# Performance work log

Hardware: AMD Instinct MI355X
Metric: run time of the kernel (lower is better)

## Reference

```python
import jax, jax.numpy as jnp
import numpy as np

N_NODES = 100000


def _sage_conv(x, src, dst, Wl, b, Wr):
    """PyG SAGEConv with mean aggregation: lin_l(mean_{j->i} x_j) + lin_r(x_i)."""
    msg = x[src]  # [E, d] gather of source-node features
    s = jax.ops.segment_sum(msg, dst, num_segments=N_NODES)  # [N, d]
    deg = jax.ops.segment_sum(jnp.ones_like(dst, dtype=x.dtype), dst,
                              num_segments=N_NODES)  # [N]
    mean = s / jnp.maximum(deg, 1.0)[:, None]  # nodes with no in-edges -> 0
    return mean @ Wl.T + b + x @ Wr.T


def setup_inputs() -> dict:
    key = jax.random.key(0)
    ks = jax.random.split(key, 12)
    in_f, h_f, out_f = 64, 64, 32
    E_half = 800000
    x = jax.random.normal(ks[0], (N_NODES, in_f), dtype=jnp.float32)
    edge_index1 = jax.random.randint(ks[1], (2, E_half), 0, N_NODES, dtype=jnp.int64)
    edge_weight1 = jax.random.uniform(ks[2], (E_half,), dtype=jnp.float32)
    edge_index2 = jax.random.randint(ks[3], (2, E_half), 0, N_NODES, dtype=jnp.int64)
    edge_weight2 = jax.random.uniform(ks[4], (E_half,), dtype=jnp.float32)
    s1 = 1.0 / np.sqrt(in_f)
    s2 = 1.0 / np.sqrt(h_f)
    W1l = jax.random.uniform(ks[5], (h_f, in_f), minval=-s1, maxval=s1, dtype=jnp.float32)
    b1 = jax.random.uniform(ks[6], (h_f,), minval=-s1, maxval=s1, dtype=jnp.float32)
    W1r = jax.random.uniform(ks[7], (h_f, in_f), minval=-s1, maxval=s1, dtype=jnp.float32)
    W2l = jax.random.uniform(ks[8], (out_f, h_f), minval=-s2, maxval=s2, dtype=jnp.float32)
    b2 = jax.random.uniform(ks[9], (out_f,), minval=-s2, maxval=s2, dtype=jnp.float32)
    W2r = jax.random.uniform(ks[10], (out_f, h_f), minval=-s2, maxval=s2, dtype=jnp.float32)
    return {"x": x, "edge_index1": edge_index1, "edge_weight1": edge_weight1,
            "edge_index2": edge_index2, "edge_weight2": edge_weight2,
            "W1l": W1l, "b1": b1, "W1r": W1r, "W2l": W2l, "b2": b2, "W2r": W2r}


def reference(x, edge_index1, edge_weight1, edge_index2, edge_weight2,
              W1l, b1, W1r, W2l, b2, W2r):
    # concat adjacency lists (edge_weight is concatenated but unused by SAGEConv)
    edge_index = jnp.concatenate([edge_index1, edge_index2], axis=-1)
    _edge_weight = jnp.concatenate([edge_weight1, edge_weight2], axis=-1)  # unused
    src, dst = edge_index[0], edge_index[1]
    # F.dropout with training=False -> identity (eval-mode reference)
    h = _sage_conv(x, src, dst, W1l, b1, W1r)
    h = jax.nn.relu(h)
    out = _sage_conv(h, src, dst, W2l, b2, W2r)
    return out
```

## Files before the change

### kernel.cpp

```cpp
#include <hip/hip_runtime.h>


constexpr int N_NODES = 100000;
constexpr int E_HALF  = 800000;
constexpr int E_TOT   = 2 * E_HALF;
constexpr int CAP     = 64;
constexpr int OVF_CAP = 4096;
constexpr int NB      = 200;
constexpr int NPB     = 500;
constexpr int BCAP    = 12288;
constexpr int EPB_A   = 2048;
constexpr int EPT_A   = EPB_A / 256;
constexpr int BINA_BLKS   = (E_TOT + EPB_A - 1) / EPB_A;
constexpr int CONV_BLKS   = N_NODES * 64 / 4 / 256;
constexpr int WSPLIT_BLKS = 48;

typedef short  s16x8 __attribute__((ext_vector_type(8)));
typedef float  f32x4 __attribute__((ext_vector_type(4)));
typedef unsigned short u16;

__device__ inline float bf(u16 u) { return __uint_as_float(((unsigned)u) << 16); }
__device__ inline u16 f2bf(float v) {
    unsigned b = __float_as_uint(v);
    b += 0x7FFFu + ((b >> 16) & 1u);
    return (u16)(b >> 16);
}
__device__ inline void acc4(float* s, uint2 v) {
    s[0] += __uint_as_float(v.x << 16);
    s[1] += __uint_as_float(v.x & 0xFFFF0000u);
    s[2] += __uint_as_float(v.y << 16);
    s[3] += __uint_as_float(v.y & 0xFFFF0000u);
}

__global__ __launch_bounds__(256) void binA_kernel(
    const int* __restrict__ ei1, const int* __restrict__ ei2,
    const float* __restrict__ x, u16* __restrict__ xb,
    const float* __restrict__ W1l, const float* __restrict__ W1r,
    const float* __restrict__ W2l, const float* __restrict__ W2r,
    short* __restrict__ B1hi, short* __restrict__ B1lo,
    short* __restrict__ B2hi, short* __restrict__ B2lo,
    uint2* __restrict__ barr, int* __restrict__ bcur,
    int* __restrict__ ovfA_cnt, int* __restrict__ ovfA)
{
    __shared__ int   hist[NB], base[NB], cur[NB], lofs[NB];
    __shared__ int   scan[256];
    __shared__ int   aux[EPB_A];
    __shared__ uint2 staged[EPB_A];
    int tid = threadIdx.x;

    if (blockIdx.x >= BINA_BLKS) {
        int bx = blockIdx.x - BINA_BLKS;
        if (bx < CONV_BLKS) {
            int i = bx * 256 + tid;
            float4 v = ((const float4*)x)[i];
            ushort4 rr;
            rr.x = f2bf(v.x); rr.y = f2bf(v.y);
            rr.z = f2bf(v.z); rr.w = f2bf(v.w);
            ((ushort4*)xb)[i] = rr;
        } else {
            int i = (bx - CONV_BLKS) * 256 + tid;
            float v; short* ph; short* pl; int idx;
            if (i < 64 * 128) {
                int o = i >> 7, k = i & 127;
                v = (k < 64) ? W1l[o * 64 + k] : W1r[o * 64 + (k - 64)];
                ph = B1hi; pl = B1lo; idx = i;
            } else {
                int j = i - 64 * 128;
                int o = j >> 6, k = j & 63;
                v = (o < 32) ? W2l[o * 64 + k] : W2r[(o - 32) * 64 + k];
                ph = B2hi; pl = B2lo; idx = j;
            }
            unsigned b  = __float_as_uint(v);
            float    hf = __uint_as_float(b & 0xFFFF0000u);
            float    r  = v - hf;
            ph[idx] = (short)(b >> 16);
            pl[idx] = (short)(__float_as_uint(r) >> 16);
        }
        return;
    }

    for (int t = tid; t < NB; t += 256) { hist[t] = 0; cur[t] = 0; }
    __syncthreads();

    int e0 = blockIdx.x * EPB_A;
    uint2 myE[EPT_A];
    int   myB[EPT_A];
    #pragma unroll
    for (int k = 0; k < EPT_A; k++) {
        int e = e0 + k * 256 + tid;
        myB[k] = -1;
        if (e < E_TOT) {
            const int* ei = (e < E_HALF) ? ei1 : ei2;
            int ee = (e < E_HALF) ? e : e - E_HALF;
            int dst = ei[E_HALF + ee];
            int src = ei[ee];
            myE[k] = make_uint2((unsigned)src, (unsigned)dst);
            myB[k] = dst / NPB;
            atomicAdd(&hist[myB[k]], 1);
        }
    }
    __syncthreads();

    int v = (tid < NB) ? hist[tid] : 0;
    scan[tid] = v;
    __syncthreads();
    #pragma unroll
    for (int off = 1; off < 256; off <<= 1) {
        int u = (tid >= off) ? scan[tid - off] : 0;
        __syncthreads();
        scan[tid] += u;
        __syncthreads();
    }
    if (tid < NB) lofs[tid] = scan[tid] - v;
    if (tid < NB) base[tid] = atomicAdd(&bcur[tid], hist[tid]);
    __syncthreads();

    #pragma unroll
    for (int k = 0; k < EPT_A; k++) {
        int b = myB[k];
        if (b < 0) continue;
        int rank = atomicAdd(&cur[b], 1);
        int p    = lofs[b] + rank;
        int gpos = base[b] + rank;
        if (gpos < BCAP) {
            staged[p] = myE[k];
            aux[p]    = b * BCAP + gpos;
        } else {
            aux[p] = -1;
            int o = atomicAdd(ovfA_cnt, 1);
            if (o < OVF_CAP) {
                ovfA[2 * o] = (int)myE[k].x; ovfA[2 * o + 1] = (int)myE[k].y;
            }
        }
    }
    __syncthreads();

    int tot = scan[255];
    for (int i = tid; i < tot; i += 256) {
        int a = aux[i];
        if (a >= 0) barr[a] = staged[i];
    }
}

__global__ __launch_bounds__(1024) void binB_kernel(
    const uint2* __restrict__ barr, const int* __restrict__ bcur,
    const int* __restrict__ ovfA_cnt, const int* __restrict__ ovfA,
    int* __restrict__ cnt, int* __restrict__ slots,
    int* __restrict__ ovfB_cnt, int* __restrict__ ovfB)
{
    __shared__ int lcnt[NPB];
    int tid = threadIdx.x, b = blockIdx.x;
    for (int t = tid; t < NPB; t += 1024) lcnt[t] = 0;
    __syncthreads();
    int nE = bcur[b]; if (nE > BCAP) nE = BCAP;
    int dbase = b * NPB;
    for (int i = tid; i < nE; i += 1024) {
        uint2 e = barr[b * BCAP + i];
        int dst = (int)e.y;
        int pos = atomicAdd(&lcnt[dst - dbase], 1);
        if (pos < CAP) {
            slots[dst * CAP + pos] = (int)e.x;
        } else {
            int o = atomicAdd(ovfB_cnt, 1);
            if (o < OVF_CAP) { ovfB[2 * o] = (int)e.x; ovfB[2 * o + 1] = dst; }
        }
    }
    __syncthreads();
    int nOA = *ovfA_cnt; if (nOA > OVF_CAP) nOA = OVF_CAP;
    for (int t = tid; t < nOA; t += 1024) {
        int src = ovfA[2 * t], dst = ovfA[2 * t + 1];
        if (dst >= dbase && dst < dbase + NPB) {
            int pos = atomicAdd(&lcnt[dst - dbase], 1);
            if (pos < CAP) {
                slots[dst * CAP + pos] = src;
            } else {
                int o = atomicAdd(ovfB_cnt, 1);
                if (o < OVF_CAP) { ovfB[2 * o] = src; ovfB[2 * o + 1] = dst; }
            }
        }
    }
    __syncthreads();
    for (int t = tid; t < NPB; t += 1024) {
        int n = dbase + t;
        if (n < N_NODES) cnt[n] = lcnt[t];
    }
}

__device__ inline void split8(float4 v0, float4 v1, s16x8& hi, s16x8& lo) {
    float vs[8] = {v0.x, v0.y, v0.z, v0.w, v1.x, v1.y, v1.z, v1.w};
    s16x8 h, l;
    #pragma unroll
    for (int j = 0; j < 8; j++) {
        unsigned b  = __float_as_uint(vs[j]);
        float    hf = __uint_as_float(b & 0xFFFF0000u);
        float    r  = vs[j] - hf;
        h[j] = (short)(b >> 16);
        l[j] = (short)(__float_as_uint(r) >> 16);
    }
    hi = h; lo = l;
}

template <int MT>
__global__ __launch_bounds__(256) void gather_gemm1_kernel(
    const u16*  __restrict__ xb,
    const float* __restrict__ x,
    const int*  __restrict__ cnt,
    const int*  __restrict__ slots,
    const int*  __restrict__ ovfB_cnt, const int* __restrict__ ovfB,
    const short* __restrict__ Bhi, const short* __restrict__ Blo,
    const float* __restrict__ bias, u16* __restrict__ hb)
{
    constexpr int RPW = MT * 16;
    __shared__ float ldsA[4][RPW][66];
    const int widx = threadIdx.x >> 6;
    const int lane = threadIdx.x & 63;
    const int m0   = (blockIdx.x * 4 + widx) * RPW;
    const int r = lane >> 4;
    const int c = lane & 15;

    int pdA, pdB, psvA, psvB;
    {
        int nA = m0, nB = m0 + 1;
        pdA  = (nA < N_NODES) ? cnt[nA] : 0;
        pdB  = (nB < N_NODES) ? cnt[nB] : 0;
        psvA = (nA < N_NODES) ? slots[nA * CAP + lane] : 0;
        psvB = (nB < N_NODES) ? slots[nB * CAP + lane] : 0;
    }
    #pragma unroll 1
    for (int j = 0; j < RPW; j += 2) {
        const int dA = pdA, dB = pdB;
        const int rsvA = psvA, rsvB = psvB;
        if (j + 2 < RPW) {
            int nA = m0 + j + 2, nB = m0 + j + 3;
            pdA  = (nA < N_NODES) ? cnt[nA] : 0;
            pdB  = (nB < N_NODES) ? cnt[nB] : 0;
            psvA = (nA < N_NODES) ? slots[nA * CAP + lane] : 0;
            psvB = (nB < N_NODES) ? slots[nB * CAP + lane] : 0;
        }
        const int cA = dA < CAP ? dA : CAP;
        const int cB = dB < CAP ? dB : CAP;
        const int svA = (lane < cA) ? rsvA : 0;
        const int svB = (lane < cB) ? rsvB : 0;
        float sA[16], sB[16];
        #pragma unroll
        for (int k = 0; k < 16; k++) { sA[k] = 0.f; sB[k] = 0.f; }
        const int cM = cA > cB ? cA : cB;
        for (int i = 0; i < cM; i += 16) {
            const int i0 = i + r, i1 = i + 4 + r, i2 = i + 8 + r, i3 = i + 12 + r;
            int tA0 = __shfl(svA, i0 & 63), tA1 = __shfl(svA, i1 & 63),
                tA2 = __shfl(svA, i2 & 63), tA3 = __shfl(svA, i3 & 63);
            int tB0 = __shfl(svB, i0 & 63), tB1 = __shfl(svB, i1 & 63),
                tB2 = __shfl(svB, i2 & 63), tB3 = __shfl(svB, i3 & 63);
            uint2 vA0 = make_uint2(0u, 0u), vA1 = vA0, vA2 = vA0, vA3 = vA0;
            uint2 vB0 = vA0, vB1 = vA0, vB2 = vA0, vB3 = vA0;
            if (i0 < cA) vA0 = *(const uint2*)&xb[tA0 * 64 + c * 4];
            if (i1 < cA) vA1 = *(const uint2*)&xb[tA1 * 64 + c * 4];
            if (i2 < cA) vA2 = *(const uint2*)&xb[tA2 * 64 + c * 4];
            if (i3 < cA) vA3 = *(const uint2*)&xb[tA3 * 64 + c * 4];
            if (i0 < cB) vB0 = *(const uint2*)&xb[tB0 * 64 + c * 4];
            if (i1 < cB) vB1 = *(const uint2*)&xb[tB1 * 64 + c * 4];
            if (i2 < cB) vB2 = *(const uint2*)&xb[tB2 * 64 + c * 4];
            if (i3 < cB) vB3 = *(const uint2*)&xb[tB3 * 64 + c * 4];
            acc4(&sA[0], vA0); acc4(&sA[4],  vA1);
            acc4(&sA[8], vA2); acc4(&sA[12], vA3);
            acc4(&sB[0], vB0); acc4(&sB[4],  vB1);
            acc4(&sB[8], vB2); acc4(&sB[12], vB3);
        }
        #pragma unroll
        for (int k = 0; k < 4; k++) {
            float fA = sA[k] + sA[k + 4] + sA[k + 8] + sA[k + 12];
            float fB = sB[k] + sB[k + 4] + sB[k + 8] + sB[k + 12];
            fA += __shfl_xor(fA, 16); fA += __shfl_xor(fA, 32);
            fB += __shfl_xor(fB, 16); fB += __shfl_xor(fB, 32);
            sA[k] = fA; sB[k] = fB;
        }
        if (r == 0) {
            const float rdA = 1.0f / fmaxf((float)dA, 1.0f);
            const float rdB = 1.0f / fmaxf((float)dB, 1.0f);
            float2* pA = (float2*)&ldsA[widx][j][c * 4];
            float2* pB = (float2*)&ldsA[widx][j + 1][c * 4];
            pA[0] = make_float2(sA[0] * rdA, sA[1] * rdA);
            pA[1] = make_float2(sA[2] * rdA, sA[3] * rdA);
            pB[0] = make_float2(sB[0] * rdB, sB[1] * rdB);
            pB[1] = make_float2(sB[2] * rdB, sB[3] * rdB);
        }
    }
    __syncthreads();

    {
        int nOv = *ovfB_cnt; if (nOv > OVF_CAP) nOv = OVF_CAP;
        for (int t = 0; t < nOv; ++t) {
            int src = ovfB[2 * t], dst = ovfB[2 * t + 1];
            if (dst >= m0 && dst < m0 + RPW && dst < N_NODES) {
                float rd = 1.0f / fmaxf((float)cnt[dst], 1.0f);
                ldsA[widx][dst - m0][lane] += bf(xb[src * 64 + lane]) * rd;
            }
        }
    }
    __syncthreads();

    f32x4 acc[MT][4];
    #pragma unroll
    for (int mt = 0; mt < MT; mt++)
        #pragma unroll
        for (int nt = 0; nt < 4; nt++) acc[mt][nt] = (f32x4)0.0f;

    #pragma unroll
    for (int half = 0; half < 2; half++) {
        #pragma unroll
        for (int sub = 0; sub < 2; sub++) {
            const int kf = sub * 32 + r * 8;
            const int kc = half * 64 + kf;
            s16x8 ahi[MT], alo[MT];
            #pragma unroll
            for (int mt = 0; mt < MT; mt++) {
                if (half == 0) {
                    const float2* p = (const float2*)&ldsA[widx][mt * 16 + c][kf];
                    float2 q0 = p[0], q1 = p[1], q2 = p[2], q3 = p[3];
                    split8(make_float4(q0.x, q0.y, q1.x, q1.y),
                           make_float4(q2.x, q2.y, q3.x, q3.y),
                           ahi[mt], alo[mt]);
                } else {
                    int row = m0 + mt * 16 + c;
                    row = row < N_NODES ? row : N_NODES - 1;
                    const float4* p = (const float4*)&x[row * 64 + kf];
                    split8(p[0], p[1], ahi[mt], alo[mt]);
                }
            }
            #pragma unroll
            for (int nt = 0; nt < 4; nt++) {
                const int n = nt * 16 + c;
                s16x8 bh = *(const s16x8*)&Bhi[n * 128 + kc];
                s16x8 bl = *(const s16x8*)&Blo[n * 128 + kc];
                #pragma unroll
                for (int mt = 0; mt < MT; mt++) {
                    acc[mt][nt] = __builtin_amdgcn_mfma_f32_16x16x32_bf16(ahi[mt], bh, acc[mt][nt], 0, 0, 0);
                    acc[mt][nt] = __builtin_amdgcn_mfma_f32_16x16x32_bf16(alo[mt], bh, acc[mt][nt], 0, 0, 0);
                    acc[mt][nt] = __builtin_amdgcn_mfma_f32_16x16x32_bf16(ahi[mt], bl, acc[mt][nt], 0, 0, 0);
                    acc[mt][nt] = __builtin_amdgcn_mfma_f32_16x16x32_bf16(alo[mt], bl, acc[mt][nt], 0, 0, 0);
                }
            }
        }
    }
    #pragma unroll
    for (int nt = 0; nt < 4; nt++) {
        float bv = bias[nt * 16 + c];
        #pragma unroll
        for (int mt = 0; mt < MT; mt++)
            #pragma unroll
            for (int rr = 0; rr < 4; rr++) {
                int row = m0 + mt * 16 + r * 4 + rr;
                if (row < N_NODES)
                    hb[row * 64 + nt * 16 + c] =
                        f2bf(fmaxf(acc[mt][nt][rr] + bv, 0.0f));
            }
    }
}

template <int MT>
__global__ __launch_bounds__(256) void gemm2_kernel(
    const u16* __restrict__ hb,
    const short* __restrict__ Bhi, const short* __restrict__ Blo,
    const float* __restrict__ b2,
    u16* __restrict__ y2b, float* __restrict__ z)
{
    int wave = (blockIdx.x * 256 + threadIdx.x) >> 6;
    int lane = threadIdx.x & 63;
    int m0   = wave * (MT * 16);
    if (m0 >= N_NODES) return;
    int quad = lane >> 4, l16 = lane & 15;

    f32x4 acc[MT][4];
    #pragma unroll
    for (int mt = 0; mt < MT; mt++)
        #pragma unroll
        for (int nt = 0; nt < 4; nt++) acc[mt][nt] = (f32x4)0.0f;

    #pragma unroll
    for (int sub = 0; sub < 2; sub++) {
        int kf = sub * 32 + quad * 8;
        s16x8 a[MT];
        #pragma unroll
        for (int mt = 0; mt < MT; mt++) {
            int row = m0 + mt * 16 + l16;
            row = row < N_NODES ? row : N_NODES - 1;
            a[mt] = *(const s16x8*)&hb[row * 64 + kf];
        }
        #pragma unroll
        for (int nt = 0; nt < 4; nt++) {
            int n = nt * 16 + l16;
            s16x8 bh = *(const s16x8*)&Bhi[n * 64 + kf];
            s16x8 bl = *(const s16x8*)&Blo[n * 64 + kf];
            #pragma unroll
            for (int mt = 0; mt < MT; mt++) {
                acc[mt][nt] = __builtin_amdgcn_mfma_f32_16x16x32_bf16(a[mt], bh, acc[mt][nt], 0, 0, 0);
                acc[mt][nt] = __builtin_amdgcn_mfma_f32_16x16x32_bf16(a[mt], bl, acc[mt][nt], 0, 0, 0);
            }
        }
    }
    #pragma unroll
    for (int nt = 0; nt < 4; nt++) {
        bool  isz = nt >= 2;
        int   col = (isz ? nt - 2 : nt) * 16 + l16;
        float bv  = isz ? b2[col] : 0.0f;
        #pragma unroll
        for (int mt = 0; mt < MT; mt++)
            #pragma unroll
            for (int r = 0; r < 4; r++) {
                int row = m0 + mt * 16 + quad * 4 + r;
                if (row < N_NODES) {
                    float v = acc[mt][nt][r] + bv;
                    if (isz) z[row * 32 + col] = v;
                    else     y2b[row * 32 + col] = f2bf(v);
                }
            }
    }
}

__global__ __launch_bounds__(256) void gather_mean32_kernel(
    const u16*  __restrict__ y2b,
    const float* __restrict__ z,
    const int*  __restrict__ cnt,
    const int*  __restrict__ slots,
    const int*  __restrict__ ovfB_cnt, const int* __restrict__ ovfB,
    float*      __restrict__ out)
{
    int node = blockIdx.x * 4 + (threadIdx.x >> 6);
    int lane = threadIdx.x & 63;
    int r    = lane >> 3;
    int c    = lane & 7;
    if (node >= N_NODES) return;
    int nOv = *ovfB_cnt; if (nOv > OVF_CAP) nOv = OVF_CAP;
    int cdeg = cnt[node];
    int cc   = cdeg < CAP ? cdeg : CAP;
    int slotv = (lane < cc) ? slots[node * CAP + lane] : 0;
    float s[16];
    #pragma unroll
    for (int k = 0; k < 16; k++) s[k] = 0.f;
    for (int i = 0; i < cc; i += 32) {
        int i0 = i + r, i1 = i + 8 + r, i2 = i + 16 + r, i3 = i + 24 + r;
        int t0 = __shfl(slotv, i0), t1 = __shfl(slotv, i1),
            t2 = __shfl(slotv, i2), t3 = __shfl(slotv, i3);
        uint2 v0 = make_uint2(0u, 0u), v1 = v0, v2 = v0, v3 = v0;
        if (i0 < cc) v0 = *(const uint2*)&y2b[t0 * 32 + c * 4];
        if (i1 < cc) v1 = *(const uint2*)&y2b[t1 * 32 + c * 4];
        if (i2 < cc) v2 = *(const uint2*)&y2b[t2 * 32 + c * 4];
        if (i3 < cc) v3 = *(const uint2*)&y2b[t3 * 32 + c * 4];
        acc4(&s[0], v0); acc4(&s[4], v1); acc4(&s[8], v2); acc4(&s[12], v3);
    }
    #pragma unroll
    for (int k = 0; k < 4; k++) {
        float f = s[k] + s[k + 4] + s[k + 8] + s[k + 12];
        f += __shfl_xor(f, 8); f += __shfl_xor(f, 16); f += __shfl_xor(f, 32);
        s[k] = f;
    }
    for (int t = 0; t < nOv; ++t) {
        int src = ovfB[2 * t], dst = ovfB[2 * t + 1];
        if (dst == node) {
            uint2 v = *(const uint2*)&y2b[src * 32 + c * 4];
            s[0] += __uint_as_float(v.x << 16);
            s[1] += __uint_as_float(v.x & 0xFFFF0000u);
            s[2] += __uint_as_float(v.y << 16);
            s[3] += __uint_as_float(v.y & 0xFFFF0000u);
        }
    }
    if (r == 0) {
        float rd = 1.0f / fmaxf((float)cdeg, 1.0f);
        float4 zz = *(const float4*)&z[node * 32 + c * 4];
        *(float4*)&out[node * 32 + c * 4] = make_float4(
            s[0] * rd + zz.x, s[1] * rd + zz.y,
            s[2] * rd + zz.z, s[3] * rd + zz.w);
    }
}

extern "C" void kernel_launch(void* const* d_in, const int* in_sizes, int n_in,
                              void* d_out, int out_size, void* d_ws, size_t ws_size,
                              hipStream_t stream) {
    const float* x   = (const float*)d_in[0];
    const int*   ei1 = (const int*)d_in[1];
    const int*   ei2 = (const int*)d_in[3];
    const float* W1l = (const float*)d_in[5];
    const float* b1  = (const float*)d_in[6];
    const float* W1r = (const float*)d_in[7];
    const float* W2l = (const float*)d_in[8];
    const float* b2  = (const float*)d_in[9];
    const float* W2r = (const float*)d_in[10];
    float* out = (float*)d_out;

    const size_t off_misc  = 400128;
    const size_t off_ovfAc = off_misc + 0;
    const size_t off_ovfBc = off_misc + 4;
    const size_t off_bcur  = off_misc + 256;
    const size_t off_ovfA  = off_misc + 1280;
    const size_t off_ovfB  = off_misc + 1280 + 8 * OVF_CAP;
    const size_t off_slots = 467200;
    const size_t off_m     = off_slots + (size_t)N_NODES * CAP * 4;
    const size_t off_h     = off_m + (size_t)N_NODES * 64 * 4;
    const size_t off_hb    = off_h + (size_t)N_NODES * 64 * 2;
    const size_t off_B1hi  = off_h + (size_t)N_NODES * 64 * 4;
    const size_t off_B1lo  = off_B1hi + 64 * 128 * 2;
    const size_t off_B2hi  = off_B1lo + 64 * 128 * 2;
    const size_t off_B2lo  = off_B2hi + 64 * 64 * 2;

    char*  ws     = (char*)d_ws;
    int*   cnt    = (int*)(ws + 0);
    int*   ovfA_c = (int*)(ws + off_ovfAc);
    int*   ovfB_c = (int*)(ws + off_ovfBc);
    int*   bcur   = (int*)(ws + off_bcur);
    int*   ovfA   = (int*)(ws + off_ovfA);
    int*   ovfB   = (int*)(ws + off_ovfB);
    int*   slots  = (int*)(ws + off_slots);
    uint2* barr   = (uint2*)(ws + off_m);
    u16*   xb     = (u16*)(ws + off_h);
    u16*   hb     = (u16*)(ws + off_hb);
    float* z      = (float*)(ws + off_m);
    u16*   y2b    = (u16*)(ws + off_m + (size_t)N_NODES * 32 * 4);
    short* B1hi   = (short*)(ws + off_B1hi);
    short* B1lo   = (short*)(ws + off_B1lo);
    short* B2hi   = (short*)(ws + off_B2hi);
    short* B2lo   = (short*)(ws + off_B2lo);

    hipMemsetAsync(ws + off_misc, 0, 1280, stream);

    binA_kernel<<<BINA_BLKS + CONV_BLKS + WSPLIT_BLKS, 256, 0, stream>>>(
        ei1, ei2, x, xb, W1l, W1r, W2l, W2r,
        B1hi, B1lo, B2hi, B2lo, barr, bcur, ovfA_c, ovfA);
    binB_kernel<<<NB, 1024, 0, stream>>>(
        barr, bcur, ovfA_c, ovfA, cnt, slots, ovfB_c, ovfB);

    {
        int waves  = (N_NODES + 31) / 32;
        int blocks = (waves + 3) / 4;
        gather_gemm1_kernel<2><<<blocks, 256, 0, stream>>>(
            xb, x, cnt, slots, ovfB_c, ovfB, B1hi, B1lo, b1, hb);
    }

    {
        int waves = (N_NODES + 63) / 64;
        gemm2_kernel<4><<<(waves + 3) / 4, 256, 0, stream>>>(
            hb, B2hi, B2lo, b2, y2b, z);
    }
    gather_mean32_kernel<<<N_NODES / 4, 256, 0, stream>>>(
        y2b, z, cnt, slots, ovfB_c, ovfB, out);
}
```

Measured before the change: 237.3 us.

## Move x/weight conversion into binB launch and gather two nodes per wave

The x-to-bf16 and weight hi/lo split work moves out of the edge-binning kernel and into the binB launch as extra 1024-thread blocks. There they can fill the GPU alongside the 200 bucket blocks, which on their own underuse the device. The final mean-gather kernel now has each wave process two nodes, interleaving their loads to expose more memory-level parallelism and halving the block count. The cost is higher register pressure from two accumulators, and wasted loads when the two nodes' degrees differ.

```diff
diff --git a/kernel.cpp b/kernel.cpp
--- a/kernel.cpp
+++ b/kernel.cpp
@@ -12,8 +12,9 @@
 constexpr int EPB_A   = 2048;
 constexpr int EPT_A   = EPB_A / 256;
 constexpr int BINA_BLKS   = (E_TOT + EPB_A - 1) / EPB_A;
-constexpr int CONV_BLKS   = N_NODES * 64 / 4 / 256;
-constexpr int WSPLIT_BLKS = 48;
+constexpr int CONV_ITEMS  = N_NODES * 64 / 4;
+constexpr int CONV_BLKS_B = (CONV_ITEMS + 1023) / 1024;
+constexpr int WSPLIT_BLKS_B = 12;
 
 typedef short  s16x8 __attribute__((ext_vector_type(8)));
 typedef float  f32x4 __attribute__((ext_vector_type(4)));
@@ -34,11 +35,6 @@
 
 __global__ __launch_bounds__(256) void binA_kernel(
     const int* __restrict__ ei1, const int* __restrict__ ei2,
-    const float* __restrict__ x, u16* __restrict__ xb,
-    const float* __restrict__ W1l, const float* __restrict__ W1r,
-    const float* __restrict__ W2l, const float* __restrict__ W2r,
-    short* __restrict__ B1hi, short* __restrict__ B1lo,
-    short* __restrict__ B2hi, short* __restrict__ B2lo,
     uint2* __restrict__ barr, int* __restrict__ bcur,
     int* __restrict__ ovfA_cnt, int* __restrict__ ovfA)
 {
@@ -47,38 +43,6 @@
     __shared__ int   aux[EPB_A];
     __shared__ uint2 staged[EPB_A];
     int tid = threadIdx.x;
-
-    if (blockIdx.x >= BINA_BLKS) {
-        int bx = blockIdx.x - BINA_BLKS;
-        if (bx < CONV_BLKS) {
-            int i = bx * 256 + tid;
-            float4 v = ((const float4*)x)[i];
-            ushort4 rr;
-            rr.x = f2bf(v.x); rr.y = f2bf(v.y);
-            rr.z = f2bf(v.z); rr.w = f2bf(v.w);
-            ((ushort4*)xb)[i] = rr;
-        } else {
-            int i = (bx - CONV_BLKS) * 256 + tid;
-            float v; short* ph; short* pl; int idx;
-            if (i < 64 * 128) {
-                int o = i >> 7, k = i & 127;
-                v = (k < 64) ? W1l[o * 64 + k] : W1r[o * 64 + (k - 64)];
-                ph = B1hi; pl = B1lo; idx = i;
-            } else {
-                int j = i - 64 * 128;
-                int o = j >> 6, k = j & 63;
-                v = (o < 32) ? W2l[o * 64 + k] : W2r[(o - 32) * 64 + k];
-                ph = B2hi; pl = B2lo; idx = j;
-            }
-            unsigned b  = __float_as_uint(v);
-            float    hf = __uint_as_float(b & 0xFFFF0000u);
-            float    r  = v - hf;
-            ph[idx] = (short)(b >> 16);
-            pl[idx] = (short)(__float_as_uint(r) >> 16);
-        }
-        return;
-    }
-
     for (int t = tid; t < NB; t += 256) { hist[t] = 0; cur[t] = 0; }
     __syncthreads();
 
@@ -145,11 +109,50 @@
 __global__ __launch_bounds__(1024) void binB_kernel(
     const uint2* __restrict__ barr, const int* __restrict__ bcur,
     const int* __restrict__ ovfA_cnt, const int* __restrict__ ovfA,
+    const float* __restrict__ x, u16* __restrict__ xb,
+    const float* __restrict__ W1l, const float* __restrict__ W1r,
+    const float* __restrict__ W2l, const float* __restrict__ W2r,
+    short* __restrict__ B1hi, short* __restrict__ B1lo,
+    short* __restrict__ B2hi, short* __restrict__ B2lo,
     int* __restrict__ cnt, int* __restrict__ slots,
     int* __restrict__ ovfB_cnt, int* __restrict__ ovfB)
 {
+    int tid = threadIdx.x;
+    if (blockIdx.x >= NB) {
+        int bx = blockIdx.x - NB;
+        if (bx < CONV_BLKS_B) {
+            int i = bx * 1024 + tid;
+            if (i < CONV_ITEMS) {
+                float4 v = ((const float4*)x)[i];
+                ushort4 rr;
+                rr.x = f2bf(v.x); rr.y = f2bf(v.y);
+                rr.z = f2bf(v.z); rr.w = f2bf(v.w);
+                ((ushort4*)xb)[i] = rr;
+            }
+        } else {
+            int i = (bx - CONV_BLKS_B) * 1024 + tid;
+            float v; short* ph; short* pl; int idx;
+            if (i < 64 * 128) {
+                int o = i >> 7, k = i & 127;
+                v = (k < 64) ? W1l[o * 64 + k] : W1r[o * 64 + (k - 64)];
+                ph = B1hi; pl = B1lo; idx = i;
+            } else {
+                int j = i - 64 * 128;
+                int o = j >> 6, k = j & 63;
+                v = (o < 32) ? W2l[o * 64 + k] : W2r[(o - 32) * 64 + k];
+                ph = B2hi; pl = B2lo; idx = j;
+            }
+            unsigned b  = __float_as_uint(v);
+            float    hf = __uint_as_float(b & 0xFFFF0000u);
+            float    r  = v - hf;
+            ph[idx] = (short)(b >> 16);
+            pl[idx] = (short)(__float_as_uint(r) >> 16);
+        }
+        return;
+    }
+
     __shared__ int lcnt[NPB];
-    int tid = threadIdx.x, b = blockIdx.x;
+    int b = blockIdx.x;
     for (int t = tid; t < NPB; t += 1024) lcnt[t] = 0;
     __syncthreads();
     int nE = bcur[b]; if (nE > BCAP) nE = BCAP;
@@ -425,39 +428,58 @@
     const int*  __restrict__ ovfB_cnt, const int* __restrict__ ovfB,
     float*      __restrict__ out)
 {
-    int node = blockIdx.x * 4 + (threadIdx.x >> 6);
+    int nA   = (blockIdx.x * 4 + (threadIdx.x >> 6)) * 2;
+    int nB   = nA + 1;
     int lane = threadIdx.x & 63;
     int r    = lane >> 3;
     int c    = lane & 7;
-    if (node >= N_NODES) return;
+    if (nA >= N_NODES) return;
     int nOv = *ovfB_cnt; if (nOv > OVF_CAP) nOv = OVF_CAP;
-    int cdeg = cnt[node];
-    int cc   = cdeg < CAP ? cdeg : CAP;
-    int slotv = (lane < cc) ? slots[node * CAP + lane] : 0;
-    float s[16];
-    #pragma unroll
-    for (int k = 0; k < 16; k++) s[k] = 0.f;
-    for (int i = 0; i < cc; i += 32) {
+    int dA = cnt[nA];
+    int dB = (nB < N_NODES) ? cnt[nB] : 0;
+    int cA = dA < CAP ? dA : CAP;
+    int cB = dB < CAP ? dB : CAP;
+    int svA = (lane < cA) ? slots[nA * CAP + lane] : 0;
+    int svB = (nB < N_NODES && lane < cB) ? slots[nB * CAP + lane] : 0;
+    float sA[16], sB[16];
+    #pragma unroll
+    for (int k = 0; k < 16; k++) { sA[k] = 0.f; sB[k] = 0.f; }
+    const int cM = cA > cB ? cA : cB;
+    for (int i = 0; i < cM; i += 32) {
         int i0 = i + r, i1 = i + 8 + r, i2 = i + 16 + r, i3 = i + 24 + r;
-        int t0 = __shfl(slotv, i0), t1 = __shfl(slotv, i1),
-            t2 = __shfl(slotv, i2), t3 = __shfl(slotv, i3);
-        uint2 v0 = make_uint2(0u, 0u), v1 = v0, v2 = v0, v3 = v0;
-        if (i0 < cc) v0 = *(const uint2*)&y2b[t0 * 32 + c * 4];
-        if (i1 < cc) v1 = *(const uint2*)&y2b[t1 * 32 + c * 4];
-        if (i2 < cc) v2 = *(const uint2*)&y2b[t2 * 32 + c * 4];
-        if (i3 < cc) v3 = *(const uint2*)&y2b[t3 * 32 + c * 4];
-        acc4(&s[0], v0); acc4(&s[4], v1); acc4(&s[8], v2); acc4(&s[12], v3);
+        int tA0 = __shfl(svA, i0 & 63), tA1 = __shfl(svA, i1 & 63),
+            tA2 = __shfl(svA, i2 & 63), tA3 = __shfl(svA, i3 & 63);
+        int tB0 = __shfl(svB, i0 & 63), tB1 = __shfl(svB, i1 & 63),
+            tB2 = __shfl(svB, i2 & 63), tB3 = __shfl(svB, i3 & 63);
+        uint2 z2 = make_uint2(0u, 0u);
+        uint2 vA0 = z2, vA1 = z2, vA2 = z2, vA3 = z2;
+        uint2 vB0 = z2, vB1 = z2, vB2 = z2, vB3 = z2;
+        if (i0 < cA) vA0 = *(const uint2*)&y2b[tA0 * 32 + c * 4];
+        if (i1 < cA) vA1 = *(const uint2*)&y2b[tA1 * 32 + c * 4];
+        if (i2 < cA) vA2 = *(const uint2*)&y2b[tA2 * 32 + c * 4];
+        if (i3 < cA) vA3 = *(const uint2*)&y2b[tA3 * 32 + c * 4];
+        if (i0 < cB) vB0 = *(const uint2*)&y2b[tB0 * 32 + c * 4];
+        if (i1 < cB) vB1 = *(const uint2*)&y2b[tB1 * 32 + c * 4];
+        if (i2 < cB) vB2 = *(const uint2*)&y2b[tB2 * 32 + c * 4];
+        if (i3 < cB) vB3 = *(const uint2*)&y2b[tB3 * 32 + c * 4];
+        acc4(&sA[0], vA0); acc4(&sA[4],  vA1);
+        acc4(&sA[8], vA2); acc4(&sA[12], vA3);
+        acc4(&sB[0], vB0); acc4(&sB[4],  vB1);
+        acc4(&sB[8], vB2); acc4(&sB[12], vB3);
     }
     #pragma unroll
     for (int k = 0; k < 4; k++) {
-        float f = s[k] + s[k + 4] + s[k + 8] + s[k + 12];
-        f += __shfl_xor(f, 8); f += __shfl_xor(f, 16); f += __shfl_xor(f, 32);
-        s[k] = f;
+        float fA = sA[k] + sA[k + 4] + sA[k + 8] + sA[k + 12];
+        float fB = sB[k] + sB[k + 4] + sB[k + 8] + sB[k + 12];
+        fA += __shfl_xor(fA, 8); fA += __shfl_xor(fA, 16); fA += __shfl_xor(fA, 32);
+        fB += __shfl_xor(fB, 8); fB += __shfl_xor(fB, 16); fB += __shfl_xor(fB, 32);
+        sA[k] = fA; sB[k] = fB;
     }
     for (int t = 0; t < nOv; ++t) {
         int src = ovfB[2 * t], dst = ovfB[2 * t + 1];
-        if (dst == node) {
+        if (dst == nA || dst == nB) {
             uint2 v = *(const uint2*)&y2b[src * 32 + c * 4];
+            float* s = (dst == nA) ? sA : sB;
             s[0] += __uint_as_float(v.x << 16);
             s[1] += __uint_as_float(v.x & 0xFFFF0000u);
             s[2] += __uint_as_float(v.y << 16);
@@ -465,11 +487,18 @@
         }
     }
     if (r == 0) {
-        float rd = 1.0f / fmaxf((float)cdeg, 1.0f);
-        float4 zz = *(const float4*)&z[node * 32 + c * 4];
-        *(float4*)&out[node * 32 + c * 4] = make_float4(
-            s[0] * rd + zz.x, s[1] * rd + zz.y,
-            s[2] * rd + zz.z, s[3] * rd + zz.w);
+        float rdA = 1.0f / fmaxf((float)dA, 1.0f);
+        float4 zzA = *(const float4*)&z[nA * 32 + c * 4];
+        *(float4*)&out[nA * 32 + c * 4] = make_float4(
+            sA[0] * rdA + zzA.x, sA[1] * rdA + zzA.y,
+            sA[2] * rdA + zzA.z, sA[3] * rdA + zzA.w);
+        if (nB < N_NODES) {
+            float rdB = 1.0f / fmaxf((float)dB, 1.0f);
+            float4 zzB = *(const float4*)&z[nB * 32 + c * 4];
+            *(float4*)&out[nB * 32 + c * 4] = make_float4(
+                sB[0] * rdB + zzB.x, sB[1] * rdB + zzB.y,
+                sB[2] * rdB + zzB.z, sB[3] * rdB + zzB.w);
+        }
     }
 }
 
@@ -522,11 +551,11 @@
 
     hipMemsetAsync(ws + off_misc, 0, 1280, stream);
 
-    binA_kernel<<<BINA_BLKS + CONV_BLKS + WSPLIT_BLKS, 256, 0, stream>>>(
-        ei1, ei2, x, xb, W1l, W1r, W2l, W2r,
-        B1hi, B1lo, B2hi, B2lo, barr, bcur, ovfA_c, ovfA);
-    binB_kernel<<<NB, 1024, 0, stream>>>(
-        barr, bcur, ovfA_c, ovfA, cnt, slots, ovfB_c, ovfB);
+    binA_kernel<<<BINA_BLKS, 256, 0, stream>>>(
+        ei1, ei2, barr, bcur, ovfA_c, ovfA);
+    binB_kernel<<<NB + CONV_BLKS_B + WSPLIT_BLKS_B, 1024, 0, stream>>>(
+        barr, bcur, ovfA_c, ovfA, x, xb, W1l, W1r, W2l, W2r,
+        B1hi, B1lo, B2hi, B2lo, cnt, slots, ovfB_c, ovfB);
 
     {
         int waves  = (N_NODES + 31) / 32;
@@ -540,6 +569,6 @@
         gemm2_kernel<4><<<(waves + 3) / 4, 256, 0, stream>>>(
             hb, B2hi, B2lo, b2, y2b, z);
     }
-    gather_mean32_kernel<<<N_NODES / 4, 256, 0, stream>>>(
+    gather_mean32_kernel<<<(N_NODES + 7) / 8, 256, 0, stream>>>(
         y2b, z, cnt, slots, ovfB_c, ovfB, out);
 }
```

Result: slower. 254.6 us (+7.3%).
